# Kernel optimization log

Measured on AMD Instinct MI355X. Metric: run time of the kernel, lower is better.

Reference implementation:

```python
import jax, jax.numpy as jnp
import numpy as np

DIM = 1024
HEADS = 16
DIM_HEAD = 64
INNER = HEADS * DIM_HEAD  # 1024
B, N = 4, 1024
SCALE = DIM_HEAD ** -0.5


def _layernorm(t, g, b, eps=1e-5):
    mu = jnp.mean(t, axis=-1, keepdims=True)
    var = jnp.var(t, axis=-1, keepdims=True)
    return (t - mu) * jax.lax.rsqrt(var + eps) * g + b


def setup_inputs() -> dict:
    key = jax.random.key(0)
    ks = jax.random.split(key, 8)
    return {
        "x": jax.random.normal(ks[0], (B, N, DIM), dtype=jnp.float32),
        "y": jax.random.normal(ks[1], (B, N, DIM), dtype=jnp.float32),
        "gx": jnp.ones((DIM,), jnp.float32),
        "bx": jnp.zeros((DIM,), jnp.float32),
        "gy": jnp.ones((DIM,), jnp.float32),
        "by": jnp.zeros((DIM,), jnp.float32),
        "Wqkv_x": jax.random.normal(ks[2], (DIM, 3 * INNER), jnp.float32) * 0.02,
        "Wqkv_y": jax.random.normal(ks[3], (DIM, 3 * INNER), jnp.float32) * 0.02,
        "Wout_x": jax.random.normal(ks[4], (INNER, DIM), jnp.float32) * 0.02,
        "bout_x": jnp.zeros((DIM,), jnp.float32),
        "Wout_y": jax.random.normal(ks[5], (INNER, DIM), jnp.float32) * 0.02,
        "bout_y": jnp.zeros((DIM,), jnp.float32),
    }


def _split_heads(t):
    b, n, _ = t.shape
    return t.reshape(b, n, HEADS, DIM_HEAD).transpose(0, 2, 1, 3)  # b h n d


def reference(x, y, gx, bx, gy, by, Wqkv_x, Wqkv_y, Wout_x, bout_x, Wout_y, bout_y):
    xn = _layernorm(x, gx, bx)
    yn = _layernorm(y, gy, by)
    qx, kx, vx = [_split_heads(t) for t in jnp.split(xn @ Wqkv_x, 3, axis=-1)]
    qy, ky, vy = [_split_heads(t) for t in jnp.split(yn @ Wqkv_y, 3, axis=-1)]
    # concat along HEADS dim -> 2h heads; each stream's heads attend within that stream
    q = jnp.concatenate([qx, qy], axis=1)
    k = jnp.concatenate([kx, ky], axis=1)
    v = jnp.concatenate([vx, vy], axis=1)
    dots = jnp.einsum('bhid,bhjd->bhij', q, k) * SCALE  # [B, 2h, N, N]
    attn = jax.nn.softmax(dots, axis=-1)
    out = jnp.einsum('bhij,bhjd->bhid', attn, v)  # [B, 2h, N, d]
    xo = out[:, :HEADS]  # original code uses the x-chunk for BOTH outputs (faithful)
    xo = xo.transpose(0, 2, 1, 3).reshape(xo.shape[0], xo.shape[2], INNER)  # b n (h d)
    out_x = xo @ Wout_x + bout_x
    out_y = xo @ Wout_y + bout_y
    return (out_x, out_y)
```

## Files before the change

### kernel.cpp

```cpp
#include <hip/hip_runtime.h>

typedef __attribute__((ext_vector_type(8))) short s16x8;
typedef __attribute__((ext_vector_type(4))) float f32x4;
typedef unsigned short u16;

#define DEV __device__ __forceinline__

DEV u16 f2bf(float f) {
    unsigned u = __builtin_bit_cast(unsigned, f);
    unsigned r = u + 0x7fffu + ((u >> 16) & 1u);
    return (u16)(r >> 16);
}

DEV float exp2a(float x) {
    float r;
    asm("v_exp_f32 %0, %1" : "=v"(r) : "v"(x));
    return r;
}

DEV unsigned cvtpk(float lo, float hi) {
    unsigned r;
    asm("v_cvt_pk_bf16_f32 %0, %1, %2" : "=v"(r) : "v"(lo), "v"(hi));
    return r;
}

DEV void gload_lds16(const void* g, void* l) {
    __builtin_amdgcn_global_load_lds(
        (const __attribute__((address_space(1))) unsigned int*)g,
        (__attribute__((address_space(3))) unsigned int*)l, 16, 0, 0);
}

DEV f32x4 mfma16(s16x8 a, s16x8 b, f32x4 c) {
    return __builtin_amdgcn_mfma_f32_16x16x32_bf16(a, b, c, 0, 0, 0);
}

template <int N>
DEV void vmwait() {
    asm volatile("s_waitcnt vmcnt(%0)" ::"n"(N) : "memory");
}

__global__ __launch_bounds__(256) void ln_kernel(const float* __restrict__ x,
                                                 const float* __restrict__ g,
                                                 const float* __restrict__ b,
                                                 u16* __restrict__ xn) {
    const int row = blockIdx.x, t = threadIdx.x;
    const float4 v = *(const float4*)(x + (size_t)row * 1024 + t * 4);
    float s1 = v.x + v.y + v.z + v.w;
    float s2 = v.x * v.x + v.y * v.y + v.z * v.z + v.w * v.w;
#pragma unroll
    for (int d = 1; d < 64; d <<= 1) {
        s1 += __shfl_xor(s1, d);
        s2 += __shfl_xor(s2, d);
    }
    __shared__ float red[8];
    if ((t & 63) == 0) { red[(t >> 6) * 2] = s1; red[(t >> 6) * 2 + 1] = s2; }
    __syncthreads();
    s1 = red[0] + red[2] + red[4] + red[6];
    s2 = red[1] + red[3] + red[5] + red[7];
    const float mu = s1 * (1.0f / 1024.0f);
    const float var = s2 * (1.0f / 1024.0f) - mu * mu;
    const float rs = rsqrtf(var + 1e-5f);
    const float4 gv = *(const float4*)(g + t * 4);
    const float4 bv = *(const float4*)(b + t * 4);
    ushort4 o;
    o.x = f2bf((v.x - mu) * rs * gv.x + bv.x);
    o.y = f2bf((v.y - mu) * rs * gv.y + bv.y);
    o.z = f2bf((v.z - mu) * rs * gv.z + bv.z);
    o.w = f2bf((v.w - mu) * rs * gv.w + bv.w);
    *(ushort4*)(xn + (size_t)row * 1024 + t * 4) = o;
}

__global__ __launch_bounds__(256) void transpose_w(const float* __restrict__ src0,
                                                   const float* __restrict__ src1,
                                                   u16* __restrict__ dst, int ld) {
    __shared__ float tile[64][68];
    const int t = threadIdx.x;
    const float* src = (blockIdx.z == 0) ? src0 : src1;
    u16* d0 = dst + (size_t)blockIdx.z * 1024 * 1024;
    const int n0 = blockIdx.x * 64, k0 = blockIdx.y * 64;
    const int kl = t >> 4, nl = (t & 15) * 4;
#pragma unroll
    for (int p = 0; p < 4; ++p) {
        float4 v = *(const float4*)(src + (size_t)(k0 + kl + p * 16) * ld + n0 + nl);
        tile[kl + p * 16][nl + 0] = v.x;
        tile[kl + p * 16][nl + 1] = v.y;
        tile[kl + p * 16][nl + 2] = v.z;
        tile[kl + p * 16][nl + 3] = v.w;
    }
    __syncthreads();
    const int nl2 = t >> 2, kc = (t & 3) * 16;
    __align__(16) u16 tmp[16];
#pragma unroll
    for (int j = 0; j < 16; ++j) tmp[j] = f2bf(tile[kc + j][nl2]);
    u16* d = d0 + (size_t)(n0 + nl2) * 1024 + k0 + kc;
    ((uint4*)d)[0] = ((const uint4*)tmp)[0];
    ((uint4*)d)[1] = ((const uint4*)tmp)[1];
}

__global__ __launch_bounds__(256) void transpose_v(const u16* __restrict__ V,
                                                   u16* __restrict__ Vt) {
    __shared__ u16 tile[64][72];
    const int t = threadIdx.x;
    const int j0 = blockIdx.x * 64;
    const int bh = blockIdx.y;
    const u16* src = V + (size_t)bh * 65536;
    const int jl = t >> 4, dl = (t & 15) * 4;
#pragma unroll
    for (int p = 0; p < 4; ++p) {
        ushort4 v = *(const ushort4*)(src + (size_t)(j0 + jl + p * 16) * 64 + dl);
        *(ushort4*)&tile[jl + p * 16][dl] = v;
    }
    __syncthreads();
    const int dl2 = t >> 2, jc = (t & 3) * 16;
    __align__(16) u16 tmp[16];
#pragma unroll
    for (int j = 0; j < 16; ++j) tmp[j] = tile[jc + j][dl2];
    u16* d = Vt + (size_t)bh * 65536 + (size_t)dl2 * 1024 + j0 + jc;
    ((uint4*)d)[0] = ((const uint4*)tmp)[0];
    ((uint4*)d)[1] = ((const uint4*)tmp)[1];
}

template <int BN, int WM, int EPI>
__global__ __launch_bounds__(512, 2) void gemm8(const u16* __restrict__ A,
                                                const u16* __restrict__ B,
                                                u16* __restrict__ Qb, u16* __restrict__ Kb,
                                                u16* __restrict__ Vb,
                                                const float* __restrict__ bx,
                                                const float* __restrict__ by,
                                                float* __restrict__ out, int NBX) {
    constexpr int BM = 256, WN = 8 / WM;
    constexpr int TM = BM / WM, TN = BN / WN;
    constexpr int MQ = TM / 32, NQ = TN / 32;
    constexpr int HA = TM / 2, HB = TN / 2;
    constexpr int CHA = 1024;
    constexpr int CHB = BN * 4;
    constexpr int GA = 2, GB = CHB / 512;
    constexpr int NI = 8;

    __shared__ __align__(16) u16 As[2 * 2 * CHA * 8];
    __shared__ __align__(16) u16 Bs[2 * 2 * CHB * 8];

    const int tid = threadIdx.x, lane = tid & 63;
    const int wave = tid >> 6;
    const int wm = wave / WN, wn = wave % WN;
    const int lr = lane & 15, cg = lane >> 4;

    const int nwg = NBX * 16;
    const int bid = blockIdx.x;
    const int bid2 = (bid & 7) * (nwg >> 3) + (bid >> 3);
    const int bxi = bid2 % NBX, byi = bid2 / NBX;
    const int m0 = byi * 256, n0 = bxi * BN;

    const u16* __restrict__ Ag = A + (size_t)m0 * 1024;
    const u16* __restrict__ Bg = B + (size_t)n0 * 1024;

    f32x4 acc[2 * MQ][2 * NQ] = {};

#define STG_A(b, h, t)                                                              \
    do {                                                                            \
        _Pragma("unroll") for (int u = 0; u < GA; ++u) {                            \
            const int idx = u * 512 + tid;                                          \
            const int loc = idx >> 3, pp = idx & 7;                                 \
            const int row = (loc & (HA - 1)) | ((h)*HA) | ((loc / HA) * 2 * HA);    \
            gload_lds16(Ag + (size_t)row * 1024 + (t)*64 + ((pp ^ (row & 7)) << 3), \
                        &As[(((b)*2 + (h)) * CHA + idx) * 8]);                      \
        }                                                                           \
    } while (0)
#define STG_B(b, h, t)                                                              \
    do {                                                                            \
        _Pragma("unroll") for (int u = 0; u < GB; ++u) {                            \
            const int idx = u * 512 + tid;                                          \
            const int loc = idx >> 3, pp = idx & 7;                                 \
            const int row = (loc & (HB - 1)) | ((h)*HB) | ((loc / HB) * 2 * HB);    \
            gload_lds16(Bg + (size_t)row * 1024 + (t)*64 + ((pp ^ (row & 7)) << 3), \
                        &Bs[(((b)*2 + (h)) * CHB + idx) * 8]);                      \
        }                                                                           \
    } while (0)

#define LDA(bb, lm, dst)                                                            \
    _Pragma("unroll") for (int mf = 0; mf < MQ; ++mf)                               \
        _Pragma("unroll") for (int ks = 0; ks < 2; ++ks)                            \
            dst[mf][ks] = *(const s16x8*)&As[((((bb)*2 + (lm)) * CHA) +             \
                                              (mf * 16 + lr + wm * HA) * 8 +        \
                                              ((cg + ks * 4) ^ (lr & 7))) * 8];

#define LDB(bb, ln, dst)                                                            \
    _Pragma("unroll") for (int nf = 0; nf < NQ; ++nf)                               \
        _Pragma("unroll") for (int ks = 0; ks < 2; ++ks)                            \
            dst[nf][ks] = *(const s16x8*)&Bs[((((bb)*2 + (ln)) * CHB) +             \
                                              (nf * 16 + lr + wn * HB) * 8 +        \
                                              ((cg + ks * 4) ^ (lr & 7))) * 8];

#define MM(lm, ln, A_, B_)                                                          \
    __builtin_amdgcn_s_setprio(1);                                                  \
    _Pragma("unroll") for (int mf = 0; mf < MQ; ++mf)                               \
        _Pragma("unroll") for (int nf = 0; nf < NQ; ++nf)                           \
            _Pragma("unroll") for (int ks = 0; ks < 2; ++ks)                        \
                acc[(lm)*MQ + mf][(ln)*NQ + nf] = mfma16(                           \
                    A_[mf][ks], B_[nf][ks], acc[(lm)*MQ + mf][(ln)*NQ + nf]);       \
    __builtin_amdgcn_s_setprio(0);

#define BAR() asm volatile("s_barrier" ::: "memory")

    STG_A(0, 0, 0);
    STG_A(0, 1, 0);
    STG_B(0, 0, 0);
    STG_B(0, 1, 0);
    STG_A(1, 0, 1);
    STG_B(1, 0, 1);
    vmwait<GA + GB>();
    BAR();

    s16x8 va[MQ][2];
    s16x8 vb0[NQ][2], vb1[NQ][2];

#pragma unroll 1
    for (int i = 0; i < NI - 1; ++i) {
        const int t1 = 2 * i + 1, t2 = 2 * i + 2, t3 = 2 * i + 3;
        LDA(0, 0, va); LDB(0, 0, vb0); STG_A(1, 1, t1); BAR(); MM(0, 0, va, vb0);
        LDB(0, 1, vb1);                STG_B(1, 1, t1); BAR(); MM(0, 1, va, vb1);
        LDA(0, 1, va);                 STG_A(0, 0, t2); BAR(); MM(1, 0, va, vb0);
        STG_B(0, 0, t2); vmwait<GA + GB>();             BAR(); MM(1, 1, va, vb1);
        LDA(1, 0, va); LDB(1, 0, vb0); STG_A(0, 1, t2); BAR(); MM(0, 0, va, vb0);
        LDB(1, 1, vb1);                STG_B(0, 1, t2); BAR(); MM(0, 1, va, vb1);
        LDA(1, 1, va);                 STG_A(1, 0, t3); BAR(); MM(1, 0, va, vb0);
        STG_B(1, 0, t3); vmwait<GA + GB>();             BAR(); MM(1, 1, va, vb1);
    }
    LDA(0, 0, va); LDB(0, 0, vb0); STG_A(1, 1, 15); BAR(); MM(0, 0, va, vb0);
    LDB(0, 1, vb1);                STG_B(1, 1, 15); BAR(); MM(0, 1, va, vb1);
    LDA(0, 1, va);                                  BAR(); MM(1, 0, va, vb0);
    vmwait<0>();                                    BAR(); MM(1, 1, va, vb1);
    LDA(1, 0, va); LDB(1, 0, vb0); MM(0, 0, va, vb0);
    LDB(1, 1, vb1);                MM(0, 1, va, vb1);
    LDA(1, 1, va);                 MM(1, 0, va, vb0);
    MM(1, 1, va, vb1);

#undef STG_A
#undef STG_B
#undef LDA
#undef LDB
#undef MM
#undef BAR

#pragma unroll
    for (int am = 0; am < 2 * MQ; ++am) {
        const int lm = am / MQ, mf = am % MQ;
        const int rowb = m0 + wm * TM + lm * HA + mf * 16 + cg * 4;
#pragma unroll
        for (int an = 0; an < 2 * NQ; ++an) {
            const int ln = an / NQ, nf = an % NQ;
            const int col = n0 + wn * TN + ln * HB + nf * 16 + lr;
            if (EPI == 0) {
                const int which = col >> 10, hd = col & 1023;
                const int h = hd >> 6, dd = hd & 63;
                u16* dst = (which == 0) ? Qb : (which == 1) ? Kb : Vb;
                const float sc = (which == 0) ? 0.18033688011112042f : 1.0f;
#pragma unroll
                for (int r = 0; r < 4; ++r) {
                    const int tk = rowb + r;
                    const int bb2 = tk >> 10, ii = tk & 1023;
                    dst[(size_t)(((bb2 << 4) + h) * 1024 + ii) * 64 + dd] =
                        f2bf(acc[am][an][r] * sc);
                }
            } else {
                float bias;
                float* ob;
                if (col < 1024) { bias = bx[col]; ob = out + col; }
                else { bias = by[col - 1024]; ob = out + 4194304 + (col - 1024); }
#pragma unroll
                for (int r = 0; r < 4; ++r)
                    ob[(size_t)(rowb + r) * 1024] = acc[am][an][r] + bias;
            }
        }
    }
}

__global__ __launch_bounds__(256) void attn_kernel(const u16* __restrict__ Q,
                                                   const u16* __restrict__ Kg,
                                                   const u16* __restrict__ Vt,
                                                   u16* __restrict__ xo) {
    __shared__ __align__(16) u16 Ks[3][64 * 64];
    __shared__ __align__(16) u16 Vs[3][64 * 64];
    __shared__ __align__(16) u16 Ps[4][32 * 64];
    const int tid = threadIdx.x, lane = tid & 63, w = tid >> 6;
    const int bid = blockIdx.x;
    const int bh = (bid & 7) * 8 + ((bid >> 3) & 7);
    const int qblk = bid >> 6;
    const u16* Qh = Q + (size_t)bh * 65536;
    const u16* Kh = Kg + (size_t)bh * 65536;
    const u16* Vh = Vt + (size_t)bh * 65536;
    const int lr = lane & 15, cg = lane >> 4;
    const int q0 = qblk * 128 + w * 32;
    u16* Pw = &Ps[w][0];

    s16x8 qf[2][2];
#pragma unroll
    for (int qg = 0; qg < 2; ++qg)
#pragma unroll
        for (int ks = 0; ks < 2; ++ks)
            qf[qg][ks] =
                *(const s16x8*)(Qh + (size_t)(q0 + qg * 16 + lr) * 64 + ks * 32 + cg * 8);

    f32x4 o[2][4] = {};
    float l_s[2] = {0.f, 0.f};
    float m_s[2] = {-3e38f, -3e38f};
    int ba[4];
#pragma unroll
    for (int r = 0; r < 4; ++r) ba[r] = (cg * 4 + r) * 4;

#define STAGEKV(bufi, kv0)                                                               \
    do {                                                                                 \
        _Pragma("unroll") for (int i = 0; i < 2; ++i) {                                  \
            int idx = i * 256 + tid;                                                     \
            int row = idx >> 3, p = idx & 7;                                             \
            gload_lds16(Kh + (size_t)((kv0) + row) * 64 + ((p ^ (row & 7)) << 3),        \
                        &Ks[bufi][idx * 8]);                                             \
            gload_lds16(Vh + (size_t)row * 1024 + (kv0) + ((p ^ (row & 7)) << 3),        \
                        &Vs[bufi][idx * 8]);                                             \
        }                                                                                \
    } while (0)

    STAGEKV(0, 0);
    STAGEKV(1, 64);

    int buf = 0, sbuf = 2;
    for (int t = 0; t < 16; ++t) {
        if (t == 15) { vmwait<0>(); } else { vmwait<4>(); }
        asm volatile("s_barrier" ::: "memory");
        if (t < 14) STAGEKV(sbuf, (t + 2) * 64);

        f32x4 s[2][4] = {};
#pragma unroll
        for (int fn = 0; fn < 4; ++fn) {
            const int r = fn * 16 + lr;
#pragma unroll
            for (int ks = 0; ks < 2; ++ks) {
                const int c = cg + ks * 4;
                s16x8 kf = *(const s16x8*)&Ks[buf][r * 64 + ((c ^ (r & 7)) << 3)];
                s[0][fn] = mfma16(kf, qf[0][ks], s[0][fn]);
                s[1][fn] = mfma16(kf, qf[1][ks], s[1][fn]);
            }
        }

#pragma unroll
        for (int qg = 0; qg < 2; ++qg) {
            float tm = -3e38f;
#pragma unroll
            for (int fn = 0; fn < 4; ++fn)
#pragma unroll
                for (int r = 0; r < 4; ++r) tm = fmaxf(tm, s[qg][fn][r]);
            tm = fmaxf(tm, __shfl_xor(tm, 16));
            tm = fmaxf(tm, __shfl_xor(tm, 32));
            if (!__all(tm <= m_s[qg] + 8.0f)) {
                const float mn = fmaxf(m_s[qg], tm);
                const float corr = exp2a(m_s[qg] - mn);
                m_s[qg] = mn;
                l_s[qg] *= corr;
                f32x4 corr_o;
#pragma unroll
                for (int r = 0; r < 4; ++r)
                    corr_o[r] = __builtin_bit_cast(
                        float,
                        __builtin_amdgcn_ds_bpermute(ba[r], __builtin_bit_cast(int, corr)));
#pragma unroll
                for (int fd = 0; fd < 4; ++fd) o[qg][fd] *= corr_o;
            }
            const float mn = m_s[qg];
            float rs = 0.f;
            const int prow = (qg * 16 + lr) * 64;
#pragma unroll
            for (int fn = 0; fn < 4; ++fn) {
                const float p0 = exp2a(s[qg][fn][0] - mn);
                const float p1 = exp2a(s[qg][fn][1] - mn);
                const float p2 = exp2a(s[qg][fn][2] - mn);
                const float p3 = exp2a(s[qg][fn][3] - mn);
                rs += (p0 + p1) + (p2 + p3);
                uint2 dd;
                dd.x = cvtpk(p0, p1);
                dd.y = cvtpk(p2, p3);
                *(uint2*)(Pw + prow + (((2 * fn + (cg >> 1)) ^ (lr & 7)) << 3) +
                          ((cg & 1) << 2)) = dd;
            }
            rs += __shfl_xor(rs, 16);
            rs += __shfl_xor(rs, 32);
            l_s[qg] += rs;
        }

        s16x8 pf[2][2];
#pragma unroll
        for (int qg = 0; qg < 2; ++qg)
#pragma unroll
            for (int ks = 0; ks < 2; ++ks)
                pf[qg][ks] = *(const s16x8*)(Pw + (qg * 16 + lr) * 64 +
                                             (((4 * ks + cg) ^ (lr & 7)) << 3));
#pragma unroll
        for (int fd = 0; fd < 4; ++fd) {
            const int rr = fd * 16 + lr;
#pragma unroll
            for (int ks = 0; ks < 2; ++ks) {
                const int c = cg + ks * 4;
                s16x8 vf = *(const s16x8*)&Vs[buf][rr * 64 + ((c ^ (rr & 7)) << 3)];
                o[0][fd] = mfma16(pf[0][ks], vf, o[0][fd]);
                o[1][fd] = mfma16(pf[1][ks], vf, o[1][fd]);
            }
        }
        buf = (buf == 2) ? 0 : buf + 1;
        sbuf = (sbuf == 2) ? 0 : sbuf + 1;
    }
#undef STAGEKV

    const int b = bh >> 4, h = bh & 15;
#pragma unroll
    for (int qg = 0; qg < 2; ++qg) {
        f32x4 inv;
#pragma unroll
        for (int r = 0; r < 4; ++r) {
            const float lq = __builtin_bit_cast(
                float, __builtin_amdgcn_ds_bpermute(ba[r], __builtin_bit_cast(int, l_s[qg])));
            inv[r] = 1.0f / lq;
        }
#pragma unroll
        for (int r = 0; r < 4; ++r) {
            const int qrow = q0 + qg * 16 + cg * 4 + r;
#pragma unroll
            for (int fd = 0; fd < 4; ++fd)
                xo[(size_t)(b * 1024 + qrow) * 1024 + h * 64 + fd * 16 + lr] =
                    f2bf(o[qg][fd][r] * inv[r]);
        }
    }
}

extern "C" void kernel_launch(void* const* d_in, const int* in_sizes, int n_in,
                              void* d_out, int out_size, void* d_ws, size_t ws_size,
                              hipStream_t stream) {
    const float* x = (const float*)d_in[0];
    const float* gx = (const float*)d_in[2];
    const float* bxv = (const float*)d_in[3];
    const float* Wqkv = (const float*)d_in[6];
    const float* Woutx = (const float*)d_in[8];
    const float* boutx = (const float*)d_in[9];
    const float* Wouty = (const float*)d_in[10];
    const float* bouty = (const float*)d_in[11];
    float* out = (float*)d_out;

    u16* ws = (u16*)d_ws;
    u16* xn = ws;
    u16* wqkv_t = xn + 4096 * 1024;
    u16* wout_t = wqkv_t + 3072 * 1024;
    u16* Qb = wout_t + 2048 * 1024;
    u16* Kb = Qb + 64 * 1024 * 64;
    u16* Vb = Kb + 64 * 1024 * 64;
    u16* Vtb = Vb + 64 * 1024 * 64;
    u16* xob = Vtb + 64 * 1024 * 64;

    ln_kernel<<<4096, 256, 0, stream>>>(x, gx, bxv, xn);
    transpose_w<<<dim3(48, 16, 1), 256, 0, stream>>>(Wqkv, nullptr, wqkv_t, 3072);
    transpose_w<<<dim3(16, 16, 2), 256, 0, stream>>>(Woutx, Wouty, wout_t, 1024);
    gemm8<256, 2, 0><<<192, 512, 0, stream>>>(xn, wqkv_t, Qb, Kb, Vb, nullptr, nullptr,
                                              nullptr, 12);
    transpose_v<<<dim3(16, 64), 256, 0, stream>>>(Vb, Vtb);
    attn_kernel<<<512, 256, 0, stream>>>(Qb, Kb, Vtb, xob);
    gemm8<128, 4, 1><<<256, 512, 0, stream>>>(xob, wout_t, nullptr, nullptr, nullptr,
                                              boutx, bouty, out, 16);
}
```

Measured before the change: 111.6 us.

## Use 256x192 tiles for QKV GEMM to fill all 256 CUs

Replaces the QKV projection GEMM (previously 192 blocks of 256x256 tiles) with a dedicated kernel that uses 256x192 tiles, giving 256 blocks, one per CU on MI355X. It keeps the double-buffered LDS pipeline with swizzled direct-to-LDS loads, reworked for 3 B-chunks per stage, and remaps block IDs for locality. The aim is to remove the tail imbalance of 192 blocks on 256 CUs, at the cost of lower arithmetic intensity per tile.

```diff
diff --git a/kernel.cpp b/kernel.cpp
--- a/kernel.cpp
+++ b/kernel.cpp
@@ -118,6 +118,142 @@
     u16* d = Vt + (size_t)bh * 65536 + (size_t)dl2 * 1024 + j0 + jc;
     ((uint4*)d)[0] = ((const uint4*)tmp)[0];
     ((uint4*)d)[1] = ((const uint4*)tmp)[1];
+}
+
+__global__ __launch_bounds__(512, 2) void gemm1k(const u16* __restrict__ A,
+                                                 const u16* __restrict__ B,
+                                                 u16* __restrict__ Qb, u16* __restrict__ Kb,
+                                                 u16* __restrict__ Vb) {
+    constexpr int MQ = 2, NQ = 3, HA = 32, HB = 48, TM = 64, TN = 96;
+    constexpr int CHA = 1024, CHBF = 1536;
+    constexpr int NI = 8;
+
+    __shared__ __align__(16) u16 As[2 * 2 * CHA * 8];
+    __shared__ __align__(16) u16 Bs[2 * CHBF * 8];
+
+    const int tid = threadIdx.x, lane = tid & 63;
+    const int wave = tid >> 6;
+    const int wm = wave >> 1, wn = wave & 1;
+    const int lr = lane & 15, cg = lane >> 4;
+
+    const int bid = blockIdx.x;
+    const int bid2 = (bid & 7) * 32 + (bid >> 3);
+    const int bxi = bid2 & 15, byi = bid2 >> 4;
+    const int m0 = byi * 256, n0 = bxi * 192;
+
+    const u16* __restrict__ Ag = A + (size_t)m0 * 1024;
+    const u16* __restrict__ Bg = B + (size_t)n0 * 1024;
+
+    f32x4 acc[2 * MQ][2 * NQ] = {};
+
+#define STG_A(b, h, t)                                                              \
+    do {                                                                            \
+        _Pragma("unroll") for (int u = 0; u < 2; ++u) {                             \
+            const int idx = u * 512 + tid;                                          \
+            const int loc = idx >> 3, pp = idx & 7;                                 \
+            const int row = (loc & 127) | ((h)*128);                                \
+            gload_lds16(Ag + (size_t)row * 1024 + (t)*64 + ((pp ^ (row & 7)) << 3), \
+                        &As[(((b)*2 + (h)) * CHA + idx) * 8]);                      \
+        }                                                                           \
+    } while (0)
+#define STG_B(b, t)                                                                 \
+    do {                                                                            \
+        _Pragma("unroll") for (int u = 0; u < 3; ++u) {                             \
+            const int idx = u * 512 + tid;                                          \
+            const int row = idx >> 3, pp = idx & 7;                                 \
+            gload_lds16(Bg + (size_t)row * 1024 + (t)*64 + ((pp ^ (row & 7)) << 3), \
+                        &Bs[((b)*CHBF + idx) * 8]);                                 \
+        }                                                                           \
+    } while (0)
+
+#define LDA(bb, lm, dst)                                                            \
+    _Pragma("unroll") for (int mf = 0; mf < MQ; ++mf)                               \
+        _Pragma("unroll") for (int ks = 0; ks < 2; ++ks) {                          \
+            const int grow = wm * 64 + (lm)*32 + mf * 16 + lr;                      \
+            dst[mf][ks] = *(const s16x8*)&As[((((bb)*2 + (grow >> 7)) * CHA) +      \
+                                              (grow & 127) * 8 +                    \
+                                              ((cg + ks * 4) ^ (lr & 7))) * 8];     \
+        }
+
+#define LDB(bb, ln, dst)                                                            \
+    _Pragma("unroll") for (int nf = 0; nf < NQ; ++nf)                               \
+        _Pragma("unroll") for (int ks = 0; ks < 2; ++ks) {                          \
+            const int rr = wn * TN + (ln)*HB + nf * 16 + lr;                        \
+            dst[nf][ks] = *(const s16x8*)&Bs[((bb)*CHBF + rr * 8 +                  \
+                                              ((cg + ks * 4) ^ (lr & 7))) * 8];     \
+        }
+
+#define MM(lm, ln, A_, B_)                                                          \
+    __builtin_amdgcn_s_setprio(1);                                                  \
+    _Pragma("unroll") for (int mf = 0; mf < MQ; ++mf)                               \
+        _Pragma("unroll") for (int nf = 0; nf < NQ; ++nf)                           \
+            _Pragma("unroll") for (int ks = 0; ks < 2; ++ks)                        \
+                acc[(lm)*MQ + mf][(ln)*NQ + nf] = mfma16(                           \
+                    A_[mf][ks], B_[nf][ks], acc[(lm)*MQ + mf][(ln)*NQ + nf]);       \
+    __builtin_amdgcn_s_setprio(0);
+
+#define BAR() asm volatile("s_barrier" ::: "memory")
+
+    STG_A(0, 0, 0);
+    STG_A(0, 1, 0);
+    STG_B(0, 0);
+    STG_A(1, 0, 1);
+    STG_B(1, 1);
+    vmwait<5>();
+    BAR();
+
+    s16x8 va[MQ][2];
+    s16x8 vb0[NQ][2], vb1[NQ][2];
+
+#pragma unroll 1
+    for (int i = 0; i < NI - 1; ++i) {
+        const int t1 = 2 * i + 1, t2 = 2 * i + 2, t3 = 2 * i + 3;
+        LDA(0, 0, va); LDB(0, 0, vb0); STG_A(1, 1, t1); BAR(); MM(0, 0, va, vb0);
+        LDB(0, 1, vb1);                                 BAR(); MM(0, 1, va, vb1);
+        LDA(0, 1, va);                 STG_A(0, 0, t2); BAR(); MM(1, 0, va, vb0);
+        STG_B(0, t2); vmwait<5>();                      BAR(); MM(1, 1, va, vb1);
+        LDA(1, 0, va); LDB(1, 0, vb0); STG_A(0, 1, t2); BAR(); MM(0, 0, va, vb0);
+        LDB(1, 1, vb1);                                 BAR(); MM(0, 1, va, vb1);
+        LDA(1, 1, va);                 STG_A(1, 0, t3); BAR(); MM(1, 0, va, vb0);
+        STG_B(1, t3); vmwait<5>();                      BAR(); MM(1, 1, va, vb1);
+    }
+    LDA(0, 0, va); LDB(0, 0, vb0); STG_A(1, 1, 15); BAR(); MM(0, 0, va, vb0);
+    LDB(0, 1, vb1);                                 BAR(); MM(0, 1, va, vb1);
+    LDA(0, 1, va);                                  BAR(); MM(1, 0, va, vb0);
+    vmwait<0>();                                    BAR(); MM(1, 1, va, vb1);
+    LDA(1, 0, va); LDB(1, 0, vb0); MM(0, 0, va, vb0);
+    LDB(1, 1, vb1);                MM(0, 1, va, vb1);
+    LDA(1, 1, va);                 MM(1, 0, va, vb0);
+    MM(1, 1, va, vb1);
+
+#undef STG_A
+#undef STG_B
+#undef LDA
+#undef LDB
+#undef MM
+#undef BAR
+
+#pragma unroll
+    for (int am = 0; am < 2 * MQ; ++am) {
+        const int lm = am / MQ, mf = am % MQ;
+        const int rowb = m0 + wm * TM + lm * HA + mf * 16 + cg * 4;
+#pragma unroll
+        for (int an = 0; an < 2 * NQ; ++an) {
+            const int ln = an / NQ, nf = an % NQ;
+            const int col = n0 + wn * TN + ln * HB + nf * 16 + lr;
+            const int which = col >> 10, hd = col & 1023;
+            const int h = hd >> 6, dd = hd & 63;
+            u16* dst = (which == 0) ? Qb : (which == 1) ? Kb : Vb;
+            const float sc = (which == 0) ? 0.18033688011112042f : 1.0f;
+#pragma unroll
+            for (int r = 0; r < 4; ++r) {
+                const int tk = rowb + r;
+                const int bb2 = tk >> 10, ii = tk & 1023;
+                dst[(size_t)(((bb2 << 4) + h) * 1024 + ii) * 64 + dd] =
+                    f2bf(acc[am][an][r] * sc);
+            }
+        }
+    }
 }
 
 template <int BN, int WM, int EPI>
@@ -456,8 +592,7 @@
     ln_kernel<<<4096, 256, 0, stream>>>(x, gx, bxv, xn);
     transpose_w<<<dim3(48, 16, 1), 256, 0, stream>>>(Wqkv, nullptr, wqkv_t, 3072);
     transpose_w<<<dim3(16, 16, 2), 256, 0, stream>>>(Woutx, Wouty, wout_t, 1024);
-    gemm8<256, 2, 0><<<192, 512, 0, stream>>>(xn, wqkv_t, Qb, Kb, Vb, nullptr, nullptr,
-                                              nullptr, 12);
+    gemm1k<<<256, 512, 0, stream>>>(xn, wqkv_t, Qb, Kb, Vb);
     transpose_v<<<dim3(16, 64), 256, 0, stream>>>(Vb, Vtb);
     attn_kernel<<<512, 256, 0, stream>>>(Qb, Kb, Vtb, xob);
     gemm8<128, 4, 1><<<256, 512, 0, stream>>>(xob, wout_t, nullptr, nullptr, nullptr,
```

Measured after the change: 106.1 us, median of 5. -4.9%, faster.
